# Optimization experiments

Measured on AMD Instinct MI355X. Metric: run time of the kernel, lower is better.

Reference implementation:

```python
import jax, jax.numpy as jnp
import numpy as np

K = 16  # kNN neighbors


def _knn(xb, k):
    # xb: [N, H] -> [N, k] nearest-neighbor indices (self excluded)
    sq = jnp.sum(xb * xb, axis=-1)
    d = sq[:, None] + sq[None, :] - 2.0 * (xb @ xb.T)  # squared distances [N, N]
    n = xb.shape[0]
    big = jnp.asarray(1e30, d.dtype)
    d = d + jnp.eye(n, dtype=d.dtype) * big  # mask self-loops
    _, idx = jax.lax.top_k(-d, k)
    return idx


def _edgeconv(h, W0, b0, W1, b1, k):
    # Dynamic kNN graph on current features + EdgeConv with 2-layer MLP, aggr='add'
    idx = jax.vmap(lambda xb: _knn(xb, k))(h)                 # [B, N, k]
    xj = jax.vmap(lambda xb, ib: xb[ib])(h, idx)              # [B, N, k, H] gather neighbors
    xi = jnp.broadcast_to(h[:, :, None, :], xj.shape)         # [B, N, k, H]
    m = jnp.concatenate([xi, xj - xi], axis=-1)               # [B, N, k, 2H]
    e = jax.nn.elu(m @ W0 + b0)
    e = jax.nn.elu(e @ W1 + b1)
    return jnp.sum(e, axis=2)                                 # 'add' aggregation over neighbors


def _forward(x, W_in0, b_in0, W_in1, b_in1, W_in2, b_in2,
             W_e0, b_e0, W_e1, b_e1,
             W_o0, b_o0, W_o1, b_o1, W_o2, b_o2):
    # input network (in_layers=3)
    h = jax.nn.elu(x @ W_in0 + b_in0)
    h = jax.nn.elu(h @ W_in1 + b_in1)
    h = jax.nn.elu(h @ W_in2 + b_in2)
    # agg_layers=2 blocks of dynamic-kNN EdgeConv
    for l in range(W_e0.shape[0]):
        h = _edgeconv(h, W_e0[l], b_e0[l], W_e1[l], b_e1[l], K)
    # global max pool over nodes of each graph (pool='max')
    g = jnp.max(h, axis=1)                                    # [B, H]
    # output network (out_layers=3)
    g = jax.nn.elu(g @ W_o0 + b_o0)
    g = jax.nn.elu(g @ W_o1 + b_o1)
    logits = g @ W_o2 + b_o2
    return jax.nn.log_softmax(logits, axis=1)


def setup_inputs() -> dict:
    key = jax.random.key(0)
    ks = jax.random.split(key, 8)
    B, N, F, H, C, A = 128, 512, 5, 64, 10, 2
    s = jnp.float32(0.1)

    def w(k, shape):
        return jax.random.normal(k, shape, jnp.float32) * s

    return {
        'x': jax.random.normal(ks[0], (B, N, F), jnp.float32),
        'W_in0': w(ks[1], (F, H)), 'b_in0': jnp.zeros((H,), jnp.float32),
        'W_in1': w(ks[2], (H, H)), 'b_in1': jnp.zeros((H,), jnp.float32),
        'W_in2': w(ks[3], (H, H)), 'b_in2': jnp.zeros((H,), jnp.float32),
        'W_e0': w(ks[4], (A, 2 * H, H)), 'b_e0': jnp.zeros((A, H), jnp.float32),
        'W_e1': w(ks[5], (A, H, H)), 'b_e1': jnp.zeros((A, H), jnp.float32),
        'W_o0': w(ks[6], (H, H)), 'b_o0': jnp.zeros((H,), jnp.float32),
        'W_o1': w(ks[7], (H, H)), 'b_o1': jnp.zeros((H,), jnp.float32),
        'W_o2': w(jax.random.fold_in(key, 99), (H, C)), 'b_o2': jnp.zeros((C,), jnp.float32),
    }


def reference(x, W_in0, b_in0, W_in1, b_in1, W_in2, b_in2,
              W_e0, b_e0, W_e1, b_e1,
              W_o0, b_o0, W_o1, b_o1, W_o2, b_o2):
    return _forward(x, W_in0, b_in0, W_in1, b_in1, W_in2, b_in2,
                    W_e0, b_e0, W_e1, b_e1,
                    W_o0, b_o0, W_o1, b_o1, W_o2, b_o2)
```

## Files before the change

kernel.cpp:

```cpp
#include <hip/hip_runtime.h>
#include <cmath>

typedef _Float16 f16;
typedef _Float16 f16x8 __attribute__((ext_vector_type(8)));
typedef float f32x4 __attribute__((ext_vector_type(4)));

#define B_ 128
#define N_ 512
#define H_ 64
#define K_ 16

__device__ __forceinline__ float elu_(float x) { return x > 0.f ? x : (__expf(x) - 1.f); }
__device__ __forceinline__ unsigned umin_(unsigned a, unsigned b) { return a < b ? a : b; }
__device__ __forceinline__ f32x4 mfma16(f16x8 a, f16x8 b, f32x4 c) {
    return __builtin_amdgcn_mfma_f32_16x16x32_f16(a, b, c, 0, 0, 0);
}
__device__ __forceinline__ f32x4 splat4(float v) { f32x4 r; r[0]=v; r[1]=v; r[2]=v; r[3]=v; return r; }
__device__ __forceinline__ unsigned mbcnt_(unsigned long long mask) {
    return __builtin_amdgcn_mbcnt_hi((unsigned)(mask >> 32),
           __builtin_amdgcn_mbcnt_lo((unsigned)mask, 0u));
}

__global__ __launch_bounds__(256) void mlp_kernel(const float* __restrict__ x,
        const float* __restrict__ W0, const float* __restrict__ b0,
        const float* __restrict__ W1, const float* __restrict__ b1,
        const float* __restrict__ W2, const float* __restrict__ b2,
        const float* __restrict__ We, const float* __restrict__ be,
        f16* __restrict__ hout, float* __restrict__ sqout,
        f16* __restrict__ Pout, f16* __restrict__ Qout)
{
    __shared__ f16 tile[4][16*72];
    const int lane = threadIdx.x & 63, wid = threadIdx.x >> 6;
    const int m = lane & 15, q = lane >> 4;
    const int rowbase = blockIdx.x*64 + wid*16;
    f16* tw = tile[wid];

    f16x8 af0, af1;
    {
        const float* xp = x + (size_t)(rowbase + m)*5;
        #pragma unroll
        for (int jj = 0; jj < 8; ++jj) { int k = q*8+jj; af0[jj] = (k < 5) ? (f16)xp[k] : (f16)0.f; }
    }
    f32x4 acc[4];
    #pragma unroll
    for (int t = 0; t < 4; ++t) {
        f16x8 bf;
        #pragma unroll
        for (int jj = 0; jj < 8; ++jj) { int k = q*8+jj; bf[jj] = (k < 5) ? (f16)W0[k*64 + t*16+m] : (f16)0.f; }
        acc[t] = splat4(b0[t*16+m]);
        acc[t] = mfma16(af0, bf, acc[t]);
    }
    #pragma unroll
    for (int t = 0; t < 4; ++t)
        #pragma unroll
        for (int r = 0; r < 4; ++r)
            tw[(q*4+r)*72 + t*16+m] = (f16)elu_(acc[t][r]);
    __syncthreads();
    af0 = *(const f16x8*)(tw + m*72 + q*8);
    af1 = *(const f16x8*)(tw + m*72 + q*8 + 32);
    __syncthreads();

    #pragma unroll
    for (int t = 0; t < 4; ++t) {
        f16x8 bfa, bfb;
        #pragma unroll
        for (int jj = 0; jj < 8; ++jj) {
            bfa[jj] = (f16)W1[(q*8+jj)*64 + t*16+m];
            bfb[jj] = (f16)W1[(q*8+jj+32)*64 + t*16+m];
        }
        acc[t] = splat4(b1[t*16+m]);
        acc[t] = mfma16(af0, bfa, acc[t]);
        acc[t] = mfma16(af1, bfb, acc[t]);
    }
    #pragma unroll
    for (int t = 0; t < 4; ++t)
        #pragma unroll
        for (int r = 0; r < 4; ++r)
            tw[(q*4+r)*72 + t*16+m] = (f16)elu_(acc[t][r]);
    __syncthreads();
    af0 = *(const f16x8*)(tw + m*72 + q*8);
    af1 = *(const f16x8*)(tw + m*72 + q*8 + 32);
    __syncthreads();

    #pragma unroll
    for (int t = 0; t < 4; ++t) {
        f16x8 bfa, bfb;
        #pragma unroll
        for (int jj = 0; jj < 8; ++jj) {
            bfa[jj] = (f16)W2[(q*8+jj)*64 + t*16+m];
            bfb[jj] = (f16)W2[(q*8+jj+32)*64 + t*16+m];
        }
        acc[t] = splat4(b2[t*16+m]);
        acc[t] = mfma16(af0, bfa, acc[t]);
        acc[t] = mfma16(af1, bfb, acc[t]);
    }
    float vv[4][4];
    float s[4] = {0.f,0.f,0.f,0.f};
    #pragma unroll
    for (int t = 0; t < 4; ++t)
        #pragma unroll
        for (int r = 0; r < 4; ++r) {
            float v = elu_(acc[t][r]);
            vv[t][r] = v;
            hout[(size_t)(rowbase + q*4 + r)*64 + t*16 + m] = (f16)v;
            s[r] += v*v;
        }
    #pragma unroll
    for (int off = 1; off <= 8; off <<= 1) {
        #pragma unroll
        for (int r = 0; r < 4; ++r) s[r] += __shfl_xor(s[r], off);
    }
    if (m == 0) {
        #pragma unroll
        for (int r = 0; r < 4; ++r) sqout[rowbase + q*4 + r] = s[r];
    }
    #pragma unroll
    for (int t = 0; t < 4; ++t)
        #pragma unroll
        for (int r = 0; r < 4; ++r)
            tw[(q*4+r)*72 + t*16+m] = (f16)vv[t][r];
    __syncthreads();
    af0 = *(const f16x8*)(tw + m*72 + q*8);
    af1 = *(const f16x8*)(tw + m*72 + q*8 + 32);

    f32x4 aP[4], aQ[4];
    #pragma unroll
    for (int t = 0; t < 4; ++t) { aP[t] = splat4(be[t*16+m]); aQ[t] = splat4(0.f); }
    #pragma unroll
    for (int cc = 0; cc < 2; ++cc) {
        const f16x8 afc = cc ? af1 : af0;
        #pragma unroll
        for (int t = 0; t < 4; ++t) {
            f16x8 bp, bq;
            #pragma unroll
            for (int jj = 0; jj < 8; ++jj) {
                float wa = We[(q*8+jj+32*cc)*64 + t*16+m];
                float wb = We[(q*8+jj+32*cc+64)*64 + t*16+m];
                bq[jj] = (f16)wb; bp[jj] = (f16)(wa - wb);
            }
            aP[t] = mfma16(afc, bp, aP[t]);
            aQ[t] = mfma16(afc, bq, aQ[t]);
        }
    }
    #pragma unroll
    for (int t = 0; t < 4; ++t)
        #pragma unroll
        for (int r = 0; r < 4; ++r) {
            Pout[(size_t)(rowbase + q*4 + r)*64 + t*16 + m] = (f16)aP[t][r];
            Qout[(size_t)(rowbase + q*4 + r)*64 + t*16 + m] = (f16)aQ[t][r];
        }
}

#define KIDX(row, col) ((row)*512 + ((col) ^ ((row) << 1)))

template<bool DOPQ>
__global__ __launch_bounds__(512, 8) void knn_kernel(const f16* __restrict__ hin,
        const float* __restrict__ sq, int* __restrict__ idxout,
        const float* __restrict__ We, const float* __restrict__ be,
        f16* __restrict__ Pout, f16* __restrict__ Qout)
{
    __shared__ unsigned keys[16*512];
    const int lane = threadIdx.x & 63;
    const int wid  = threadIdx.x >> 6;
    const int m = lane & 15, q = lane >> 4;
    const int b  = blockIdx.x >> 5;
    const int rt = blockIdx.x & 31;
    const int rowbase = rt*16;
    const f16* hb = hin + (size_t)b*N_*H_;
    const float* sqb = sq + b*N_;

    f16x8 af0, af1;
    {
        const f16* Ap = hb + (size_t)(rowbase + m)*64 + q*8;
        af0 = *(const f16x8*)Ap;
        af1 = *(const f16x8*)(Ap + 32);
    }
    #pragma unroll
    for (int ct = wid; ct < 32; ct += 8) {
        const int colbase = ct*16;
        const f16* Bp = hb + (size_t)(colbase + m)*64 + q*8;
        f16x8 bf0 = *(const f16x8*)Bp;
        f16x8 bf1 = *(const f16x8*)(Bp + 32);
        f32x4 acc = splat4(0.f);
        acc = mfma16(af0, bf0, acc);
        acc = mfma16(af1, bf1, acc);
        const float sc = sqb[colbase + m];
        #pragma unroll
        for (int r = 0; r < 4; ++r) {
            float d = fmaf(-2.f, acc[r], sc);
            unsigned u = __float_as_uint(d);
            u = ((int)u < 0) ? ~u : (u | 0x80000000u);
            unsigned key = (u & 0xFFFFFE00u) | (unsigned)(colbase + m);
            const int rowin = q*4 + r;
            if (colbase + m == rowbase + rowin) key = 0xFFFFFFFFu;
            keys[KIDX(rowin, colbase + m)] = key;
        }
    }
    __syncthreads();

    unsigned kk[2][8];
    #pragma unroll
    for (int rr = 0; rr < 2; ++rr) {
        const int ri = wid*2 + rr;
        *(uint4*)&kk[rr][0] = *(const uint4*)(keys + ri*512 + lane*4);
        *(uint4*)&kk[rr][4] = *(const uint4*)(keys + ri*512 + 256 + lane*4);
    }
    unsigned* scr = keys + wid*2*512;

    unsigned v[2];
    #pragma unroll
    for (int rr = 0; rr < 2; ++rr) {
        unsigned mn = kk[rr][0];
        #pragma unroll
        for (int s2 = 1; s2 < 8; ++s2) mn = umin_(mn, kk[rr][s2]);
        v[rr] = mn;
    }
    unsigned T[2] = {0u,0u};
    #pragma unroll
    for (int bit = 31; bit >= 9; --bit) {
        #pragma unroll
        for (int rr = 0; rr < 2; ++rr) {
            unsigned cand = T[rr] | (1u << bit);
            int c = __popcll(__ballot(v[rr] < cand));
            T[rr] = (c < 16) ? cand : T[rr];
        }
    }
    T[0] |= 511u; T[1] |= 511u;

    unsigned cnt[2];
    #pragma unroll
    for (int rr = 0; rr < 2; ++rr) {
        unsigned c = 0;
        #pragma unroll
        for (int s2 = 0; s2 < 8; ++s2) {
            const bool p = kk[rr][s2] <= T[rr];
            unsigned long long bal = __ballot(p);
            unsigned pos = c + mbcnt_(bal);
            if (p && pos < 64u) scr[rr*64 + pos] = kk[rr][s2];
            c += (unsigned)__popcll(bal);
        }
        cnt[rr] = c;
    }
    unsigned cval[2];
    #pragma unroll
    for (int rr = 0; rr < 2; ++rr)
        cval[rr] = (lane < (int)umin_(cnt[rr], 64u)) ? scr[rr*64 + lane] : 0xFFFFFFFFu;

    unsigned M2[2] = {0u,0u};
    #pragma unroll
    for (int bit = 31; bit >= 0; --bit) {
        #pragma unroll
        for (int rr = 0; rr < 2; ++rr) {
            unsigned cand = M2[rr] | (1u << bit);
            int c = __popcll(__ballot(cval[rr] < cand));
            M2[rr] = (c < 16) ? cand : M2[rr];
        }
    }
    #pragma unroll
    for (int rr = 0; rr < 2; ++rr) {
        const int ri = wid*2 + rr;
        int* outp = idxout + ((size_t)b*N_ + rowbase + ri)*K_;
        const bool p = cval[rr] <= M2[rr];
        unsigned rank = mbcnt_(__ballot(p));
        if (p) outp[rank] = (int)(cval[rr] & 511u);
    }

    if (DOPQ) {
        const int t = wid & 3;
        f32x4 acc = (wid < 4) ? splat4(be[t*16+m]) : splat4(0.f);
        #pragma unroll
        for (int cc = 0; cc < 2; ++cc) {
            const f16x8 afc = cc ? af1 : af0;
            f16x8 bb;
            if (wid < 4) {
                #pragma unroll
                for (int jj = 0; jj < 8; ++jj) {
                    float wa = We[(q*8+jj+32*cc)*64 + t*16+m];
                    float wb = We[(q*8+jj+32*cc+64)*64 + t*16+m];
                    bb[jj] = (f16)(wa - wb);
                }
            } else {
                #pragma unroll
                for (int jj = 0; jj < 8; ++jj)
                    bb[jj] = (f16)We[(q*8+jj+32*cc+64)*64 + t*16+m];
            }
            acc = mfma16(afc, bb, acc);
        }
        f16* outp = (wid < 4) ? Pout : Qout;
        #pragma unroll
        for (int r = 0; r < 4; ++r)
            outp[((size_t)b*N_ + rowbase + q*4 + r)*64 + t*16 + m] = (f16)acc[r];
    }
}

__global__ __launch_bounds__(256) void edge_kernel(const f16* __restrict__ P,
        const f16* __restrict__ Q, const int* __restrict__ idx,
        const float* __restrict__ W1, const float* __restrict__ b1,
        f16* __restrict__ out, float* __restrict__ sqout)
{
    const int lane = threadIdx.x & 63;
    const int wid  = threadIdx.x >> 6;
    const int m = lane & 15, q = lane >> 4;

    f16x8 bf[2][4];
    #pragma unroll
    for (int cc = 0; cc < 2; ++cc)
        #pragma unroll
        for (int t = 0; t < 4; ++t)
            #pragma unroll
            for (int jj = 0; jj < 8; ++jj)
                bf[cc][t][jj] = (f16)W1[(q*8 + jj + 32*cc)*64 + t*16 + m];
    float bcol[4];
    #pragma unroll
    for (int t = 0; t < 4; ++t) bcol[t] = b1[t*16 + m];

    const int node0 = blockIdx.x*64 + wid*16;
    for (int i = 0; i < 16; ++i) {
        const int r0 = node0 + i;
        const int j = idx[(size_t)r0*K_ + m];
        const int qrow = (r0 & ~(N_-1)) + j;
        f16x8 af[2];
        #pragma unroll
        for (int cc = 0; cc < 2; ++cc) {
            const int c0 = q*8 + 32*cc;
            f16x8 pv = *(const f16x8*)(P + (size_t)r0*64 + c0);
            f16x8 qv = *(const f16x8*)(Q + (size_t)qrow*64 + c0);
            #pragma unroll
            for (int jj = 0; jj < 8; ++jj)
                af[cc][jj] = (f16)elu_((float)pv[jj] + (float)qv[jj]);
        }
        f32x4 acc[4];
        #pragma unroll
        for (int t = 0; t < 4; ++t) acc[t] = splat4(bcol[t]);
        #pragma unroll
        for (int cc = 0; cc < 2; ++cc)
            #pragma unroll
            for (int t = 0; t < 4; ++t) acc[t] = mfma16(af[cc], bf[cc][t], acc[t]);
        float ssum = 0.f;
        #pragma unroll
        for (int t = 0; t < 4; ++t) {
            float s = elu_(acc[t][0]) + elu_(acc[t][1]) + elu_(acc[t][2]) + elu_(acc[t][3]);
            s += __shfl_xor(s, 16);
            s += __shfl_xor(s, 32);
            if (lane < 16) out[(size_t)r0*64 + t*16 + lane] = (f16)s;
            ssum += s*s;
        }
        #pragma unroll
        for (int off = 1; off <= 8; off <<= 1) ssum += __shfl_xor(ssum, off);
        if (lane == 0) sqout[r0] = ssum;
    }
}

__global__ __launch_bounds__(256) void final_kernel(const f16* __restrict__ hin,
        const float* __restrict__ Wo0, const float* __restrict__ bo0,
        const float* __restrict__ Wo1, const float* __restrict__ bo1,
        const float* __restrict__ Wo2, const float* __restrict__ bo2,
        float* __restrict__ out)
{
    __shared__ float smax[32][64];
    __shared__ float g0[64], g1[64], g2[64], part[4][64], lg[10];
    const int t = threadIdx.x;
    const int b = blockIdx.x;
    const int cg = t & 7, rg = t >> 3;

    float mx[8];
    #pragma unroll
    for (int e = 0; e < 8; ++e) mx[e] = -3.0e38f;
    #pragma unroll
    for (int i = 0; i < 16; ++i) {
        const int row = rg + i*32;
        f16x8 vv = *(const f16x8*)(hin + ((size_t)b*N_ + row)*64 + cg*8);
        #pragma unroll
        for (int e = 0; e < 8; ++e) mx[e] = fmaxf(mx[e], (float)vv[e]);
    }
    #pragma unroll
    for (int e = 0; e < 8; ++e) smax[rg][cg*8 + e] = mx[e];
    __syncthreads();
    for (int s = 16; s >= 1; s >>= 1) {
        if (rg < s) {
            #pragma unroll
            for (int e = 0; e < 8; ++e)
                smax[rg][cg*8+e] = fmaxf(smax[rg][cg*8+e], smax[rg+s][cg*8+e]);
        }
        __syncthreads();
    }
    if (t < 64) g0[t] = smax[0][t];
    __syncthreads();

    const int j = t & 63, p = t >> 6;
    {
        float a = 0.f;
        #pragma unroll
        for (int c = 0; c < 16; ++c) a += g0[p*16 + c]*Wo0[(p*16 + c)*64 + j];
        part[p][j] = a;
    }
    __syncthreads();
    if (t < 64) g1[t] = elu_(part[0][t] + part[1][t] + part[2][t] + part[3][t] + bo0[t]);
    __syncthreads();
    {
        float a = 0.f;
        #pragma unroll
        for (int c = 0; c < 16; ++c) a += g1[p*16 + c]*Wo1[(p*16 + c)*64 + j];
        part[p][j] = a;
    }
    __syncthreads();
    if (t < 64) g2[t] = elu_(part[0][t] + part[1][t] + part[2][t] + part[3][t] + bo1[t]);
    __syncthreads();
    if (t < 10) { float a = bo2[t]; for (int c = 0; c < 64; ++c) a += g2[c]*Wo2[c*10 + t]; lg[t] = a; }
    __syncthreads();
    if (t == 0) {
        float mxl = lg[0];
        for (int i = 1; i < 10; ++i) mxl = fmaxf(mxl, lg[i]);
        float s = 0.f;
        for (int i = 0; i < 10; ++i) s += expf(lg[i] - mxl);
        const float lse = mxl + logf(s);
        for (int i = 0; i < 10; ++i) out[b*10 + i] = lg[i] - lse;
    }
}

extern "C" void kernel_launch(void* const* d_in, const int* in_sizes, int n_in,
                              void* d_out, int out_size, void* d_ws, size_t ws_size,
                              hipStream_t stream) {
    const float* x     = (const float*)d_in[0];
    const float* W_in0 = (const float*)d_in[1];
    const float* b_in0 = (const float*)d_in[2];
    const float* W_in1 = (const float*)d_in[3];
    const float* b_in1 = (const float*)d_in[4];
    const float* W_in2 = (const float*)d_in[5];
    const float* b_in2 = (const float*)d_in[6];
    const float* W_e0  = (const float*)d_in[7];
    const float* b_e0  = (const float*)d_in[8];
    const float* W_e1  = (const float*)d_in[9];
    const float* b_e1  = (const float*)d_in[10];
    const float* Wo0   = (const float*)d_in[11];
    const float* bo0   = (const float*)d_in[12];
    const float* Wo1   = (const float*)d_in[13];
    const float* bo1   = (const float*)d_in[14];
    const float* Wo2   = (const float*)d_in[15];
    const float* bo2   = (const float*)d_in[16];

    char* ws = (char*)d_ws;
    f16*   hA   = (f16*)(ws);
    f16*   hB   = (f16*)(ws + 8388608);
    f16*   Pb   = (f16*)(ws + 16777216);
    f16*   Qb   = (f16*)(ws + 25165824);
    int*   idxb = (int*)(ws + 33554432);
    float* sqb  = (float*)(ws + 37748736);

    mlp_kernel<<<1024, 256, 0, stream>>>(x, W_in0, b_in0, W_in1, b_in1, W_in2, b_in2,
                                         W_e0, b_e0, hA, sqb, Pb, Qb);
    knn_kernel<false><<<4096, 512, 0, stream>>>(hA, sqb, idxb, nullptr, nullptr, nullptr, nullptr);
    edge_kernel<<<1024, 256, 0, stream>>>(Pb, Qb, idxb, W_e1, b_e1, hB, sqb);
    knn_kernel<true><<<4096, 512, 0, stream>>>(hB, sqb, idxb, W_e0 + 8192, b_e0 + 64, Pb, Qb);
    edge_kernel<<<1024, 256, 0, stream>>>(Pb, Qb, idxb, W_e1 + 4096, b_e1 + 64, hA, sqb);

    final_kernel<<<128, 256, 0, stream>>>(hA, Wo0, bo0, Wo1, bo1, Wo2, bo2, (float*)d_out);
}
```

Measured before the change: 303.8 us.

## Replace kNN second-stage radix select with max-elimination, reorder PQ, split edge grid

In the kNN kernel, the second 32-bit ballot radix select over the candidate set becomes an iterative loop. Each pass drops the current maximum with a wave shuffle reduction until 16 candidates remain. The DOPQ projection now runs before the sync and selection, and the float key transform becomes a branchless xor. The edge kernel handles 8 nodes per wave instead of 16, with twice the blocks and a launch-bounds occupancy hint. Together these aim to cut selection latency and raise parallelism. The elimination loop count depends on how many candidates exceed 16, and dropping several equal maxima at once could change results, though keys include the index so they are unique.

```diff
diff --git a/kernel.cpp b/kernel.cpp
--- a/kernel.cpp
+++ b/kernel.cpp
@@ -12,6 +12,7 @@
 
 __device__ __forceinline__ float elu_(float x) { return x > 0.f ? x : (__expf(x) - 1.f); }
 __device__ __forceinline__ unsigned umin_(unsigned a, unsigned b) { return a < b ? a : b; }
+__device__ __forceinline__ unsigned umax_(unsigned a, unsigned b) { return a > b ? a : b; }
 __device__ __forceinline__ f32x4 mfma16(f16x8 a, f16x8 b, f32x4 c) {
     return __builtin_amdgcn_mfma_f32_16x16x32_f16(a, b, c, 0, 0, 0);
 }
@@ -189,80 +190,12 @@
         for (int r = 0; r < 4; ++r) {
             float d = fmaf(-2.f, acc[r], sc);
             unsigned u = __float_as_uint(d);
-            u = ((int)u < 0) ? ~u : (u | 0x80000000u);
+            u ^= (0x80000000u | (unsigned)((int)u >> 31));
             unsigned key = (u & 0xFFFFFE00u) | (unsigned)(colbase + m);
             const int rowin = q*4 + r;
             if (colbase + m == rowbase + rowin) key = 0xFFFFFFFFu;
             keys[KIDX(rowin, colbase + m)] = key;
         }
-    }
-    __syncthreads();
-
-    unsigned kk[2][8];
-    #pragma unroll
-    for (int rr = 0; rr < 2; ++rr) {
-        const int ri = wid*2 + rr;
-        *(uint4*)&kk[rr][0] = *(const uint4*)(keys + ri*512 + lane*4);
-        *(uint4*)&kk[rr][4] = *(const uint4*)(keys + ri*512 + 256 + lane*4);
-    }
-    unsigned* scr = keys + wid*2*512;
-
-    unsigned v[2];
-    #pragma unroll
-    for (int rr = 0; rr < 2; ++rr) {
-        unsigned mn = kk[rr][0];
-        #pragma unroll
-        for (int s2 = 1; s2 < 8; ++s2) mn = umin_(mn, kk[rr][s2]);
-        v[rr] = mn;
-    }
-    unsigned T[2] = {0u,0u};
-    #pragma unroll
-    for (int bit = 31; bit >= 9; --bit) {
-        #pragma unroll
-        for (int rr = 0; rr < 2; ++rr) {
-            unsigned cand = T[rr] | (1u << bit);
-            int c = __popcll(__ballot(v[rr] < cand));
-            T[rr] = (c < 16) ? cand : T[rr];
-        }
-    }
-    T[0] |= 511u; T[1] |= 511u;
-
-    unsigned cnt[2];
-    #pragma unroll
-    for (int rr = 0; rr < 2; ++rr) {
-        unsigned c = 0;
-        #pragma unroll
-        for (int s2 = 0; s2 < 8; ++s2) {
-            const bool p = kk[rr][s2] <= T[rr];
-            unsigned long long bal = __ballot(p);
-            unsigned pos = c + mbcnt_(bal);
-            if (p && pos < 64u) scr[rr*64 + pos] = kk[rr][s2];
-            c += (unsigned)__popcll(bal);
-        }
-        cnt[rr] = c;
-    }
-    unsigned cval[2];
-    #pragma unroll
-    for (int rr = 0; rr < 2; ++rr)
-        cval[rr] = (lane < (int)umin_(cnt[rr], 64u)) ? scr[rr*64 + lane] : 0xFFFFFFFFu;
-
-    unsigned M2[2] = {0u,0u};
-    #pragma unroll
-    for (int bit = 31; bit >= 0; --bit) {
-        #pragma unroll
-        for (int rr = 0; rr < 2; ++rr) {
-            unsigned cand = M2[rr] | (1u << bit);
-            int c = __popcll(__ballot(cval[rr] < cand));
-            M2[rr] = (c < 16) ? cand : M2[rr];
-        }
-    }
-    #pragma unroll
-    for (int rr = 0; rr < 2; ++rr) {
-        const int ri = wid*2 + rr;
-        int* outp = idxout + ((size_t)b*N_ + rowbase + ri)*K_;
-        const bool p = cval[rr] <= M2[rr];
-        unsigned rank = mbcnt_(__ballot(p));
-        if (p) outp[rank] = (int)(cval[rr] & 511u);
     }
 
     if (DOPQ) {
@@ -291,9 +224,73 @@
         for (int r = 0; r < 4; ++r)
             outp[((size_t)b*N_ + rowbase + q*4 + r)*64 + t*16 + m] = (f16)acc[r];
     }
-}
-
-__global__ __launch_bounds__(256) void edge_kernel(const f16* __restrict__ P,
+    __syncthreads();
+
+    unsigned kk[2][8];
+    #pragma unroll
+    for (int rr = 0; rr < 2; ++rr) {
+        const int ri = wid*2 + rr;
+        *(uint4*)&kk[rr][0] = *(const uint4*)(keys + ri*512 + lane*4);
+        *(uint4*)&kk[rr][4] = *(const uint4*)(keys + ri*512 + 256 + lane*4);
+    }
+    unsigned* scr = keys + wid*2*512;
+
+    unsigned v[2];
+    #pragma unroll
+    for (int rr = 0; rr < 2; ++rr) {
+        unsigned mn = kk[rr][0];
+        #pragma unroll
+        for (int s2 = 1; s2 < 8; ++s2) mn = umin_(mn, kk[rr][s2]);
+        v[rr] = mn;
+    }
+    unsigned T[2] = {0u,0u};
+    #pragma unroll
+    for (int bit = 31; bit >= 9; --bit) {
+        #pragma unroll
+        for (int rr = 0; rr < 2; ++rr) {
+            unsigned cand = T[rr] | (1u << bit);
+            int c = __popcll(__ballot(v[rr] < cand));
+            T[rr] = (c < 16) ? cand : T[rr];
+        }
+    }
+    T[0] |= 511u; T[1] |= 511u;
+
+    unsigned cnt[2];
+    #pragma unroll
+    for (int rr = 0; rr < 2; ++rr) {
+        unsigned c = 0;
+        #pragma unroll
+        for (int s2 = 0; s2 < 8; ++s2) {
+            const bool p = kk[rr][s2] <= T[rr];
+            unsigned long long bal = __ballot(p);
+            unsigned pos = c + mbcnt_(bal);
+            if (p && pos < 64u) scr[rr*64 + pos] = kk[rr][s2];
+            c += (unsigned)__popcll(bal);
+        }
+        cnt[rr] = c;
+    }
+
+    #pragma unroll
+    for (int rr = 0; rr < 2; ++rr) {
+        const unsigned cc_ = umin_(cnt[rr], 64u);
+        bool act = lane < (int)cc_;
+        unsigned mv = act ? scr[rr*64 + lane] : 0u;
+        const int e = (int)cc_ - 16;
+        for (int it = 0; it < e; ++it) {
+            unsigned mx = mv;
+            #pragma unroll
+            for (int off = 1; off <= 32; off <<= 1) mx = umax_(mx, __shfl_xor(mx, off));
+            if (mv == mx) { act = false; mv = 0u; }
+        }
+        const int ri = wid*2 + rr;
+        int* outp = idxout + ((size_t)b*N_ + rowbase + ri)*K_;
+        unsigned long long bal = __ballot(act);
+        unsigned rank = mbcnt_(bal);
+        if (act) outp[rank] = (int)(mv & 511u);
+    }
+}
+
+__global__ __launch_bounds__(256, 5) void edge_kernel(const f16* __restrict__ P,
         const f16* __restrict__ Q, const int* __restrict__ idx,
         const float* __restrict__ W1, const float* __restrict__ b1,
         f16* __restrict__ out, float* __restrict__ sqout)
@@ -314,8 +311,8 @@
     #pragma unroll
     for (int t = 0; t < 4; ++t) bcol[t] = b1[t*16 + m];
 
-    const int node0 = blockIdx.x*64 + wid*16;
-    for (int i = 0; i < 16; ++i) {
+    const int node0 = blockIdx.x*32 + wid*8;
+    for (int i = 0; i < 8; ++i) {
         const int r0 = node0 + i;
         const int j = idx[(size_t)r0*K_ + m];
         const int qrow = (r0 & ~(N_-1)) + j;
@@ -450,9 +447,9 @@
     mlp_kernel<<<1024, 256, 0, stream>>>(x, W_in0, b_in0, W_in1, b_in1, W_in2, b_in2,
                                          W_e0, b_e0, hA, sqb, Pb, Qb);
     knn_kernel<false><<<4096, 512, 0, stream>>>(hA, sqb, idxb, nullptr, nullptr, nullptr, nullptr);
-    edge_kernel<<<1024, 256, 0, stream>>>(Pb, Qb, idxb, W_e1, b_e1, hB, sqb);
+    edge_kernel<<<2048, 256, 0, stream>>>(Pb, Qb, idxb, W_e1, b_e1, hB, sqb);
     knn_kernel<true><<<4096, 512, 0, stream>>>(hB, sqb, idxb, W_e0 + 8192, b_e0 + 64, Pb, Qb);
-    edge_kernel<<<1024, 256, 0, stream>>>(Pb, Qb, idxb, W_e1 + 4096, b_e1 + 64, hA, sqb);
+    edge_kernel<<<2048, 256, 0, stream>>>(Pb, Qb, idxb, W_e1 + 4096, b_e1 + 64, hA, sqb);
 
     final_kernel<<<128, 256, 0, stream>>>(hA, Wo0, bo0, Wo1, bo1, Wo2, bo2, (float*)d_out);
 }
```

Result: no change. 301.3 us (-0.8%).
